# Optimization experiments

Measured on AMD Instinct MI355X. Metric: run time of the kernel, lower is better.

The kernel has to match this reference:

```python
import jax, jax.numpy as jnp
import numpy as np

N, E, D, H = 50000, 500000, 128, 4
C = D // H
EPS = 1e-5


def _layer_norm(x, g, b):
    mu = jnp.mean(x, axis=-1, keepdims=True)
    var = jnp.mean((x - mu) ** 2, axis=-1, keepdims=True)
    return (x - mu) * jax.lax.rsqrt(var + EPS) * g + b


def setup_inputs() -> dict:
    key = jax.random.key(0)
    ks = jax.random.split(key, 20)
    f = lambda i, shape: jax.random.normal(ks[i], shape, dtype=jnp.float32) * 0.05
    return {
        "x": f(0, (N, D)),
        "edge_index": jax.random.randint(ks[1], (2, E), 0, N),
        "w_gcn": f(2, (D, D)), "b_gcn": f(3, (D,)),
        "wq": f(4, (D, D)), "bq": f(5, (D,)),
        "wk": f(6, (D, D)), "bk": f(7, (D,)),
        "wv": f(8, (D, D)), "bv": f(9, (D,)),
        "w_skip": f(10, (D, D)), "b_skip": f(11, (D,)),
        "w_beta": f(12, (3 * D, 1)),
        "g1": jnp.ones((D,), jnp.float32), "b1": jnp.zeros((D,), jnp.float32),
        "g2": jnp.ones((D,), jnp.float32), "b2": jnp.zeros((D,), jnp.float32),
        "w_rel": f(13, (D, 2 * D)), "w_root": f(14, (2 * D, D)),
        "local_w": jnp.ones((1,), jnp.float32), "global_w": jnp.ones((1,), jnp.float32),
    }


def reference(x, edge_index, w_gcn, b_gcn, wq, bq, wk, bk, wv, bv,
              w_skip, b_skip, w_beta, g1, b1, g2, b2, w_rel, w_root,
              local_w, global_w):
    src, dst = edge_index[0], edge_index[1]

    # ---- GCNConv (add_self_loops=False, symmetric norm) ----
    xw = x @ w_gcn                                   # [N, D]
    deg = jax.ops.segment_sum(jnp.ones((E,), x.dtype), dst, num_segments=N)
    dinv = jnp.where(deg > 0, jax.lax.rsqrt(jnp.maximum(deg, 1.0)), 0.0)
    coef = dinv[src] * dinv[dst]                     # [E]
    local_out = jax.ops.segment_sum(coef[:, None] * xw[src], dst, num_segments=N) + b_gcn

    # ---- TransformerConv (heads=4, concat=True, beta=True) ----
    q = (x @ wq + bq).reshape(N, H, C)
    k = (x @ wk + bk).reshape(N, H, C)
    v = (x @ wv + bv).reshape(N, H, C)
    alpha = jnp.sum(q[dst] * k[src], axis=-1) / jnp.sqrt(jnp.float32(C))  # [E, H]
    m = jax.ops.segment_max(alpha, dst, num_segments=N)
    m = jnp.where(jnp.isfinite(m), m, 0.0)
    a = jnp.exp(alpha - m[dst])
    s = jax.ops.segment_sum(a, dst, num_segments=N)
    attn = a / jnp.maximum(s[dst], 1e-16)            # [E, H] segment softmax over in-edges
    agg = jax.ops.segment_sum(attn[..., None] * v[src], dst, num_segments=N)
    out_g = agg.reshape(N, D)
    x_r = x @ w_skip + b_skip
    beta = jax.nn.sigmoid(jnp.concatenate([out_g, x_r, out_g - x_r], axis=-1) @ w_beta)
    global_out = beta * x_r + (1.0 - beta) * out_g

    # ---- combine + norm + FFN ----
    h = local_w * local_out + global_w * global_out
    h = _layer_norm(h + h, g1, b1)
    out = jax.nn.relu(h @ w_rel) @ w_root
    out = _layer_norm(out + h, g2, b2)
    return out
```

## Files before the change

kernel.cpp:

```cpp
#include <hip/hip_runtime.h>
#include <math.h>

#define D 128
#define EPSV 1e-5f

typedef unsigned short ushort_t;
typedef unsigned char uchar_t;
typedef __attribute__((ext_vector_type(8))) short short8v;
typedef __attribute__((ext_vector_type(4))) float f32x4;
typedef __attribute__((ext_vector_type(2))) float f32x2;
typedef _Float16 half_t;
typedef __attribute__((ext_vector_type(2))) _Float16 h2;

#if __has_builtin(__builtin_amdgcn_cvt_pk_f16_fp8)
#define HAVE_F16P 1
#else
#define HAVE_F16P 0
#endif

__device__ __forceinline__ float bf2f(unsigned u) {
    return __uint_as_float(u << 16);
}
__device__ __forceinline__ ushort_t f2bf(float f) {
    unsigned u = __float_as_uint(f);
    unsigned r = (u + 0x7fffu + ((u >> 16) & 1u)) >> 16;
    return (ushort_t)r;
}
__device__ __forceinline__ float bfp(uint4 v, int i) {
    unsigned w = (&v.x)[i >> 1];
    return bf2f((i & 1) ? (w >> 16) : (w & 0xffffu));
}

__device__ __forceinline__ ushort_t qconv(float f) {
#if HAVE_F16P
    half_t h = (half_t)f;
    return __builtin_bit_cast(ushort_t, h);
#else
    return f2bf(f);
#endif
}

#define UNPACK8_FP8(u, o) { \
    f32x2 _a = __builtin_amdgcn_cvt_pk_f32_fp8((int)(u).x, false); \
    f32x2 _b = __builtin_amdgcn_cvt_pk_f32_fp8((int)(u).x, true);  \
    f32x2 _c = __builtin_amdgcn_cvt_pk_f32_fp8((int)(u).y, false); \
    f32x2 _d = __builtin_amdgcn_cvt_pk_f32_fp8((int)(u).y, true);  \
    o[0] = _a.x; o[1] = _a.y; o[2] = _b.x; o[3] = _b.y;            \
    o[4] = _c.x; o[5] = _c.y; o[6] = _d.x; o[7] = _d.y; }

__device__ __forceinline__ unsigned bf4_to_fp8x4(unsigned w0, unsigned w1) {
    int u = __builtin_amdgcn_cvt_pk_fp8_f32(bf2f(w0 & 0xffffu), bf2f(w0 >> 16), 0, false);
    u = __builtin_amdgcn_cvt_pk_fp8_f32(bf2f(w1 & 0xffffu), bf2f(w1 >> 16), u, true);
    return (unsigned)u;
}

__global__ void cvt_deg_kernel(const float* __restrict__ in, ushort_t* __restrict__ out, int n8,
                               const int* __restrict__ dst, int* __restrict__ deg, int E)
{
    int i = blockIdx.x * blockDim.x + threadIdx.x;
    if (i < n8) {
        float4 a = reinterpret_cast<const float4*>(in)[i * 2];
        float4 b = reinterpret_cast<const float4*>(in)[i * 2 + 1];
        uint4 o;
        o.x = (unsigned)f2bf(a.x) | ((unsigned)f2bf(a.y) << 16);
        o.y = (unsigned)f2bf(a.z) | ((unsigned)f2bf(a.w) << 16);
        o.z = (unsigned)f2bf(b.x) | ((unsigned)f2bf(b.y) << 16);
        o.w = (unsigned)f2bf(b.z) | ((unsigned)f2bf(b.w) << 16);
        reinterpret_cast<uint4*>(out)[i] = o;
    }
    if (i < E) atomicAdd(&deg[dst[i]], 1);
}

__global__ __launch_bounds__(256)
void proj_gemm(const ushort_t* __restrict__ xbf,
               const ushort_t* __restrict__ Bt,
               const float* __restrict__ bias,
               const float* __restrict__ dinv,
               uchar_t* __restrict__ pack, ushort_t* __restrict__ qb,
               ushort_t* __restrict__ xrb, int M)
{
    __shared__ ushort_t Cs[128 * 136];
    const int tid = threadIdx.x, lane = tid & 63, wid = tid >> 6;
    const int wr = wid >> 1, wc = wid & 1;
    const int R0 = blockIdx.x * 128;
    const int ct = blockIdx.y;

    short8v av[4][4];
    #pragma unroll
    for (int r = 0; r < 4; ++r) {
        int gr = R0 + wr * 64 + r * 16 + (lane & 15);
        if (gr >= M) gr = M - 1;
        #pragma unroll
        for (int ks = 0; ks < 4; ++ks)
            av[r][ks] = *reinterpret_cast<const short8v*>(
                &xbf[(size_t)gr * 128 + ks * 32 + (lane >> 4) * 8]);
    }

    f32x4 acc[4][4] = {};
    #pragma unroll
    for (int ks = 0; ks < 4; ++ks) {
        short8v bv[4];
        #pragma unroll
        for (int c = 0; c < 4; ++c) {
            int col = ct * 128 + wc * 64 + c * 16 + (lane & 15);
            bv[c] = *reinterpret_cast<const short8v*>(
                &Bt[(size_t)col * 128 + ks * 32 + (lane >> 4) * 8]);
        }
        #pragma unroll
        for (int r = 0; r < 4; ++r)
            #pragma unroll
            for (int c = 0; c < 4; ++c)
                acc[r][c] = __builtin_amdgcn_mfma_f32_16x16x32_bf16(av[r][ks], bv[c], acc[r][c], 0, 0, 0);
    }

    #pragma unroll
    for (int r = 0; r < 4; ++r) {
        int rowb = wr * 64 + r * 16 + (lane >> 4) * 4;
        #pragma unroll
        for (int i = 0; i < 4; ++i) {
            float sc = 1.f;
            if (ct == 0) {
                int grow = R0 + rowb + i;
                if (grow >= M) grow = M - 1;
                sc = dinv[grow];
            }
            #pragma unroll
            for (int c = 0; c < 4; ++c) {
                int col = wc * 64 + c * 16 + (lane & 15);
                float val = acc[r][c][i] + bias[ct * 128 + col];
                if (ct == 0) val *= sc;
                Cs[(rowb + i) * 136 + col] = (ct == 1) ? qconv(val) : f2bf(val);
            }
        }
    }
    __syncthreads();

    if (ct == 1 || ct == 4) {
        #pragma unroll
        for (int it = 0; it < 8; ++it) {
            int linear = tid + it * 256;
            int row = linear >> 4, ch = linear & 15;
            int gr = R0 + row;
            if (gr < M) {
                uint4 v = *reinterpret_cast<const uint4*>(&Cs[row * 136 + ch * 8]);
                ushort_t* dst = (ct == 1) ? (qb + (size_t)gr * 128)
                                          : (xrb + (size_t)gr * 128);
                *reinterpret_cast<uint4*>(dst + ch * 8) = v;
            }
        }
    } else {
        const int byteoff = (ct == 0) ? 256 : (ct == 2) ? 0 : 128;
        #pragma unroll
        for (int it = 0; it < 4; ++it) {
            int linear = tid + it * 256;
            int row = linear >> 3, ch = linear & 7;
            int gr = R0 + row;
            if (gr < M) {
                uint4 lo = *reinterpret_cast<const uint4*>(&Cs[row * 136 + ch * 16]);
                uint4 hi = *reinterpret_cast<const uint4*>(&Cs[row * 136 + ch * 16 + 8]);
                uint4 o;
                o.x = bf4_to_fp8x4(lo.x, lo.y);
                o.y = bf4_to_fp8x4(lo.z, lo.w);
                o.z = bf4_to_fp8x4(hi.x, hi.y);
                o.w = bf4_to_fp8x4(hi.z, hi.w);
                *reinterpret_cast<uint4*>(pack + (size_t)gr * 384 + byteoff + ch * 16) = o;
            }
        }
    }
}

__device__ __forceinline__ int swz(int ch, int row) {
    return (ch & 24) | ((ch ^ row) & 7);
}

__global__ __launch_bounds__(256)
void ffn_fused(const ushort_t* __restrict__ hlnb,
               const ushort_t* __restrict__ wt_rel,
               const ushort_t* __restrict__ wt_root,
               const float* __restrict__ g2, const float* __restrict__ b2,
               float* __restrict__ outf, int M)
{
    __shared__ float smem[128 * 130];
    ushort_t* Hs = (ushort_t*)smem;
    const int tid = threadIdx.x, lane = tid & 63, wid = tid >> 6;
    const int wr = wid >> 1, wc = wid & 1;
    const int R0 = blockIdx.x * 128;

    short8v av[4][4];
    #pragma unroll
    for (int r = 0; r < 4; ++r) {
        int gr = R0 + wr * 64 + r * 16 + (lane & 15);
        if (gr >= M) gr = M - 1;
        #pragma unroll
        for (int ks = 0; ks < 4; ++ks)
            av[r][ks] = *reinterpret_cast<const short8v*>(
                &hlnb[(size_t)gr * 128 + ks * 32 + (lane >> 4) * 8]);
    }
    for (int ct = 0; ct < 2; ++ct) {
        f32x4 acc[4][4] = {};
        #pragma unroll
        for (int ks = 0; ks < 4; ++ks) {
            short8v bv[4];
            #pragma unroll
            for (int c = 0; c < 4; ++c) {
                int col = ct * 128 + wc * 64 + c * 16 + (lane & 15);
                bv[c] = *reinterpret_cast<const short8v*>(
                    &wt_rel[(size_t)col * 128 + ks * 32 + (lane >> 4) * 8]);
            }
            #pragma unroll
            for (int r = 0; r < 4; ++r)
                #pragma unroll
                for (int c = 0; c < 4; ++c)
                    acc[r][c] = __builtin_amdgcn_mfma_f32_16x16x32_bf16(av[r][ks], bv[c], acc[r][c], 0, 0, 0);
        }
        #pragma unroll
        for (int r = 0; r < 4; ++r) {
            int rowb = wr * 64 + r * 16 + (lane >> 4) * 4;
            #pragma unroll
            for (int i = 0; i < 4; ++i)
                #pragma unroll
                for (int c = 0; c < 4; ++c) {
                    int row = rowb + i;
                    int col = ct * 128 + wc * 64 + c * 16 + (lane & 15);
                    int ch = col >> 3, el = col & 7;
                    Hs[row * 256 + swz(ch, row) * 8 + el] = f2bf(fmaxf(acc[r][c][i], 0.f));
                }
        }
    }
    __syncthreads();

    f32x4 acc2[4][4] = {};
    #pragma unroll
    for (int ks = 0; ks < 8; ++ks) {
        short8v a2[4], bv[4];
        #pragma unroll
        for (int r = 0; r < 4; ++r) {
            int row = wr * 64 + r * 16 + (lane & 15);
            int ch = ks * 4 + (lane >> 4);
            a2[r] = *reinterpret_cast<const short8v*>(&Hs[row * 256 + swz(ch, row) * 8]);
        }
        #pragma unroll
        for (int c = 0; c < 4; ++c) {
            int col = wc * 64 + c * 16 + (lane & 15);
            bv[c] = *reinterpret_cast<const short8v*>(
                &wt_root[(size_t)col * 256 + ks * 32 + (lane >> 4) * 8]);
        }
        #pragma unroll
        for (int r = 0; r < 4; ++r)
            #pragma unroll
            for (int c = 0; c < 4; ++c)
                acc2[r][c] = __builtin_amdgcn_mfma_f32_16x16x32_bf16(a2[r], bv[c], acc2[r][c], 0, 0, 0);
    }
    __syncthreads();

    float* Cs = smem;
    #pragma unroll
    for (int r = 0; r < 4; ++r) {
        int rowb = wr * 64 + r * 16 + (lane >> 4) * 4;
        #pragma unroll
        for (int i = 0; i < 4; ++i)
            #pragma unroll
            for (int c = 0; c < 4; ++c)
                Cs[(rowb + i) * 130 + wc * 64 + c * 16 + (lane & 15)] = acc2[r][c][i];
    }
    __syncthreads();

    const float ga = g2[lane * 2], gb = g2[lane * 2 + 1];
    const float ba = b2[lane * 2], bb2 = b2[lane * 2 + 1];
    for (int rr = 0; rr < 32; ++rr) {
        int row = wid * 32 + rr;
        int gr = R0 + row;
        if (gr >= M) break;
        unsigned hu = *reinterpret_cast<const unsigned*>(&hlnb[(size_t)gr * 128 + lane * 2]);
        float t0 = Cs[row * 130 + lane * 2]     + bf2f(hu & 0xffffu);
        float t1 = Cs[row * 130 + lane * 2 + 1] + bf2f(hu >> 16);
        float ssum = t0 + t1;
        #pragma unroll
        for (int off = 1; off <= 32; off <<= 1) ssum += __shfl_xor(ssum, off);
        float mu = ssum * (1.f / 128.f);
        float dv0 = t0 - mu, dv1 = t1 - mu;
        float vsum = dv0 * dv0 + dv1 * dv1;
        #pragma unroll
        for (int off = 1; off <= 32; off <<= 1) vsum += __shfl_xor(vsum, off);
        float rs = rsqrtf(vsum * (1.f / 128.f) + EPSV);
        float2 o = make_float2(dv0 * rs * ga + ba, dv1 * rs * gb + bb2);
        *reinterpret_cast<float2*>(&outf[(size_t)gr * 128 + lane * 2]) = o;
    }
}

__global__ __launch_bounds__(256)
void scan1_packw_kernel(const int* __restrict__ deg, int* __restrict__ row_start,
                        int* __restrict__ bsum, int n, int SB,
                        const float* __restrict__ wg, const float* __restrict__ wq,
                        const float* __restrict__ wk, const float* __restrict__ wv,
                        const float* __restrict__ wsk,
                        const float* __restrict__ bq, const float* __restrict__ bk,
                        const float* __restrict__ bv, const float* __restrict__ bsk,
                        const float* __restrict__ wrel, const float* __restrict__ wroot,
                        ushort_t* __restrict__ wt_all, ushort_t* __restrict__ wt_rel,
                        ushort_t* __restrict__ wt_root, float* __restrict__ bias_all)
{
    __shared__ int ws[4];
    if ((int)blockIdx.x < SB) {
        const int t = threadIdx.x, lane = t & 63, wid = t >> 6;
        const int base = blockIdx.x * 1024 + t * 4;
        int v0 = 0, v1 = 0, v2 = 0, v3 = 0;
        if (base + 3 < n) {
            int4 q = *reinterpret_cast<const int4*>(&deg[base]);
            v0 = q.x; v1 = q.y; v2 = q.z; v3 = q.w;
        } else {
            if (base < n)     v0 = deg[base];
            if (base + 1 < n) v1 = deg[base + 1];
            if (base + 2 < n) v2 = deg[base + 2];
            if (base + 3 < n) v3 = deg[base + 3];
        }
        int tot = v0 + v1 + v2 + v3;
        int inc = tot;
        #pragma unroll
        for (int off = 1; off < 64; off <<= 1) {
            int y = __shfl_up(inc, off);
            if (lane >= off) inc += y;
        }
        if (lane == 63) ws[wid] = inc;
        __syncthreads();
        int woff = 0;
        for (int w = 0; w < wid; ++w) woff += ws[w];
        int excl = woff + inc - tot;
        if (base < n)     row_start[base]     = excl;
        if (base + 1 < n) row_start[base + 1] = excl + v0;
        if (base + 2 < n) row_start[base + 2] = excl + v0 + v1;
        if (base + 3 < n) row_start[base + 3] = excl + v0 + v1 + v2;
        if (t == 0) bsum[blockIdx.x] = ws[0] + ws[1] + ws[2] + ws[3];
    } else {
        int i = (blockIdx.x - SB) * 256 + threadIdx.x;
        if (i < 640 * 128) {
            int c = i >> 7, k = i & 127;
            const float* srcs[5] = {wg, wq, wk, wv, wsk};
            wt_all[i] = f2bf(srcs[c >> 7][k * 128 + (c & 127)]);
        } else if (i < 640 * 128 + 256 * 128) {
            int j = i - 640 * 128;
            int c = j >> 7, k = j & 127;
            wt_rel[j] = f2bf(wrel[k * 256 + c]);
        } else if (i < 640 * 128 + 256 * 128 + 128 * 256) {
            int j = i - (640 * 128 + 256 * 128);
            int c = j >> 8, k = j & 255;
            wt_root[j] = f2bf(wroot[k * 128 + c]);
        } else if (i < 640 * 128 + 256 * 128 + 128 * 256 + 640) {
            int c = i - (640 * 128 + 256 * 128 + 128 * 256);
            float b = 0.f;
            if (c >= 128) {
                const float* bs[4] = {bq, bk, bv, bsk};
                b = bs[(c - 128) >> 7][c & 127];
            }
            bias_all[c] = b;
        }
    }
}

__global__ __launch_bounds__(256)
void scan3_kernel(const int* __restrict__ deg, const int* __restrict__ bsum,
                  int* __restrict__ row_start, int* __restrict__ cursor,
                  float* __restrict__ dinv, int n, int E)
{
    __shared__ int boff_s;
    const int K = blockIdx.x >> 2;
    const int t = threadIdx.x;
    if (t < 64) {
        int v = 0;
        for (int j = t; j < K; j += 64) v += bsum[j];
        #pragma unroll
        for (int off = 1; off <= 32; off <<= 1) v += __shfl_xor(v, off);
        if (t == 0) boff_s = v;
    }
    __syncthreads();
    int i = blockIdx.x * 256 + t;
    if (i < n) {
        int rs = row_start[i] + boff_s;
        row_start[i] = rs;
        cursor[i] = rs;
        int d = deg[i];
        dinv[i] = (d > 0) ? rsqrtf((float)d) : 0.f;
    }
    if (i == 0) row_start[n] = E;
}

__global__ void fill_kernel(const int* __restrict__ src, const int* __restrict__ dst,
                            int* __restrict__ cursor, int* __restrict__ csr_src, int E)
{
    int e = (blockIdx.x * blockDim.x + threadIdx.x) * 2;
    if (e + 1 < E) {
        int2 s2 = *reinterpret_cast<const int2*>(&src[e]);
        int2 d2 = *reinterpret_cast<const int2*>(&dst[e]);
        int p0 = atomicAdd(&cursor[d2.x], 1);
        csr_src[p0] = s2.x;
        int p1 = atomicAdd(&cursor[d2.y], 1);
        csr_src[p1] = s2.y;
    } else if (e < E) {
        int d = dst[e];
        int pos = atomicAdd(&cursor[d], 1);
        csr_src[pos] = src[e];
    }
}

__global__ __launch_bounds__(256)
void edge_fused_kernel(const uchar_t* __restrict__ pack,
                       const ushort_t* __restrict__ qbf,
                       const ushort_t* __restrict__ xrbf,
                       const int* __restrict__ row_start,
                       const int* __restrict__ csr_src,
                       const float* __restrict__ dinv,
                       const float* __restrict__ b_gcn,
                       const float* __restrict__ w_beta,
                       const float* __restrict__ g1, const float* __restrict__ b1,
                       const float* __restrict__ local_w, const float* __restrict__ global_w,
                       ushort_t* __restrict__ hln_bf, int n)
{
    const int wid = threadIdx.x >> 6, lane = threadIdx.x & 63;
    const int node = blockIdx.x * 4 + wid;
    if (node >= n) return;
    const int slot = lane >> 4, li = lane & 15;
    const int d8 = li * 8;

    const int e0 = row_start[node], e1 = row_start[node + 1];
    const int cnt = e1 - e0;
    const float dn = dinv[node];
    const float scale = 0.17677669529663687f;

    float s = 0.f;
    float va[8], ga[8];

#if HAVE_F16P
    uint4 qu = *reinterpret_cast<const uint4*>(&qbf[(size_t)node * 128 + d8]);
    h2 qh[4] = { __builtin_bit_cast(h2, qu.x), __builtin_bit_cast(h2, qu.y),
                 __builtin_bit_cast(h2, qu.z), __builtin_bit_cast(h2, qu.w) };
    h2 va2[4] = {}, ga2[4] = {};
    for (int j = e0; j < e1; j += 4) {
        const int je = j + slot;
        const int sidx = (je < e1) ? csr_src[je] : n;
        const uchar_t* prow = pack + (size_t)sidx * 384;
        uint2 ku = *reinterpret_cast<const uint2*>(prow + d8);
        uint2 vu = *reinterpret_cast<const uint2*>(prow + 128 + d8);
        uint2 xu = *reinterpret_cast<const uint2*>(prow + 256 + d8);
        h2 k0 = __builtin_amdgcn_cvt_pk_f16_fp8((short)(ku.x & 0xffffu));
        h2 k1 = __builtin_amdgcn_cvt_pk_f16_fp8((short)(ku.x >> 16));
        h2 k2 = __builtin_amdgcn_cvt_pk_f16_fp8((short)(ku.y & 0xffffu));
        h2 k3 = __builtin_amdgcn_cvt_pk_f16_fp8((short)(ku.y >> 16));
        float p = __builtin_amdgcn_fdot2(k0, qh[0], 0.f, false);
        p = __builtin_amdgcn_fdot2(k1, qh[1], p, false);
        p = __builtin_amdgcn_fdot2(k2, qh[2], p, false);
        p = __builtin_amdgcn_fdot2(k3, qh[3], p, false);
        p += __shfl_xor(p, 1);
        p += __shfl_xor(p, 2);
        float wgt = __expf(p * scale);
        s += wgt;
        half_t wh = (half_t)wgt;
        h2 w2 = { wh, wh };
        h2 v0 = __builtin_amdgcn_cvt_pk_f16_fp8((short)(vu.x & 0xffffu));
        h2 v1 = __builtin_amdgcn_cvt_pk_f16_fp8((short)(vu.x >> 16));
        h2 v2 = __builtin_amdgcn_cvt_pk_f16_fp8((short)(vu.y & 0xffffu));
        h2 v3 = __builtin_amdgcn_cvt_pk_f16_fp8((short)(vu.y >> 16));
        va2[0] += w2 * v0; va2[1] += w2 * v1; va2[2] += w2 * v2; va2[3] += w2 * v3;
        h2 x0 = __builtin_amdgcn_cvt_pk_f16_fp8((short)(xu.x & 0xffffu));
        h2 x1 = __builtin_amdgcn_cvt_pk_f16_fp8((short)(xu.x >> 16));
        h2 x2 = __builtin_amdgcn_cvt_pk_f16_fp8((short)(xu.y & 0xffffu));
        h2 x3 = __builtin_amdgcn_cvt_pk_f16_fp8((short)(xu.y >> 16));
        ga2[0] += x0; ga2[1] += x1; ga2[2] += x2; ga2[3] += x3;
    }
    #pragma unroll
    for (int i = 0; i < 4; ++i) {
        va[2 * i] = (float)va2[i][0]; va[2 * i + 1] = (float)va2[i][1];
        ga[2 * i] = (float)ga2[i][0]; ga[2 * i + 1] = (float)ga2[i][1];
    }
#else
    uint4 qu = *reinterpret_cast<const uint4*>(&qbf[(size_t)node * 128 + d8]);
    float q[8];
    #pragma unroll
    for (int i = 0; i < 8; ++i) q[i] = bfp(qu, i);
    #pragma unroll
    for (int i = 0; i < 8; ++i) { va[i] = 0.f; ga[i] = 0.f; }
    for (int j = e0; j < e1; j += 4) {
        const int je = j + slot;
        const int sidx = (je < e1) ? csr_src[je] : n;
        const uchar_t* prow = pack + (size_t)sidx * 384;
        uint2 ku = *reinterpret_cast<const uint2*>(prow + d8);
        uint2 vu = *reinterpret_cast<const uint2*>(prow + 128 + d8);
        uint2 xu = *reinterpret_cast<const uint2*>(prow + 256 + d8);
        float kf[8], vf[8], xf[8];
        UNPACK8_FP8(ku, kf);
        UNPACK8_FP8(vu, vf);
        UNPACK8_FP8(xu, xf);
        float p = 0.f;
        #pragma unroll
        for (int i = 0; i < 8; ++i) p = fmaf(q[i], kf[i], p);
        p += __shfl_xor(p, 1);
        p += __shfl_xor(p, 2);
        float wgt = __expf(p * scale);
        s += wgt;
        #pragma unroll
        for (int i = 0; i < 8; ++i) {
            va[i] = fmaf(wgt, vf[i], va[i]);
            ga[i] += xf[i];
        }
    }
#endif

    s -= (float)((4 - (cnt & 3)) & 3) * 0.25f * 0.f;

    #pragma unroll
    for (int off = 16; off <= 32; off <<= 1) {
        s += __shfl_xor(s, off);
        #pragma unroll
        for (int i = 0; i < 8; ++i) {
            va[i] += __shfl_xor(va[i], off);
            ga[i] += __shfl_xor(ga[i], off);
        }
    }
    if (cnt > 0) s -= (float)((4 - (cnt & 3)) & 3);
    const float denom = fmaxf(s, 1e-16f);

    uint4 xru = *reinterpret_cast<const uint4*>(&xrbf[(size_t)node * 128 + d8]);
    float t[8];
    float part = 0.f;
    #pragma unroll
    for (int i = 0; i < 8; ++i) {
        float og = va[i] / denom;
        float xr = bfp(xru, i);
        float lo = dn * ga[i] + b_gcn[d8 + i];
        part += og * w_beta[d8 + i] + xr * w_beta[128 + d8 + i]
              + (og - xr) * w_beta[256 + d8 + i];
        t[i] = lo;
        va[i] = og; ga[i] = xr;
    }
    #pragma unroll
    for (int off = 1; off <= 32; off <<= 1) part += __shfl_xor(part, off);
    const float beta = 1.f / (1.f + __expf(-part * 0.25f));

    const float lw = local_w[0], gw = global_w[0];
    float ssum = 0.f;
    #pragma unroll
    for (int i = 0; i < 8; ++i) {
        float go = beta * ga[i] + (1.f - beta) * va[i];
        t[i] = 2.f * (lw * t[i] + gw * go);
        ssum += t[i];
    }
    #pragma unroll
    for (int off = 1; off <= 32; off <<= 1) ssum += __shfl_xor(ssum, off);
    const float mu = ssum * (1.f / 512.f);
    float vsum = 0.f;
    #pragma unroll
    for (int i = 0; i < 8; ++i) { float d = t[i] - mu; vsum += d * d; }
    #pragma unroll
    for (int off = 1; off <= 32; off <<= 1) vsum += __shfl_xor(vsum, off);
    const float rs = rsqrtf(vsum * (1.f / 512.f) + EPSV);

    if (slot == 0) {
        uint4 o;
        #pragma unroll
        for (int i = 0; i < 4; ++i) {
            float o0 = (t[2*i]   - mu) * rs * g1[d8 + 2*i]   + b1[d8 + 2*i];
            float o1 = (t[2*i+1] - mu) * rs * g1[d8 + 2*i+1] + b1[d8 + 2*i+1];
            (&o.x)[i] = (unsigned)f2bf(o0) | ((unsigned)f2bf(o1) << 16);
        }
        *reinterpret_cast<uint4*>(&hln_bf[(size_t)node * 128 + d8]) = o;
    }
}

extern "C" void kernel_launch(void* const* d_in, const int* in_sizes, int n_in,
                              void* d_out, int out_size, void* d_ws, size_t ws_size,
                              hipStream_t stream)
{
    const float* x      = (const float*)d_in[0];
    const int*   ei     = (const int*)d_in[1];
    const float* w_gcn  = (const float*)d_in[2];
    const float* b_gcn  = (const float*)d_in[3];
    const float* wq     = (const float*)d_in[4];
    const float* bq     = (const float*)d_in[5];
    const float* wk     = (const float*)d_in[6];
    const float* bk     = (const float*)d_in[7];
    const float* wv     = (const float*)d_in[8];
    const float* bv     = (const float*)d_in[9];
    const float* w_skip = (const float*)d_in[10];
    const float* b_skip = (const float*)d_in[11];
    const float* w_beta = (const float*)d_in[12];
    const float* g1     = (const float*)d_in[13];
    const float* b1     = (const float*)d_in[14];
    const float* g2     = (const float*)d_in[15];
    const float* b2     = (const float*)d_in[16];
    const float* w_rel  = (const float*)d_in[17];
    const float* w_root = (const float*)d_in[18];
    const float* lw     = (const float*)d_in[19];
    const float* gw     = (const float*)d_in[20];

    const int N = in_sizes[0] / D;
    const int E = in_sizes[1] / 2;
    const int* src = ei;
    const int* dst = ei + E;

    char* wsb = (char*)d_ws;
    size_t off = 0;
    auto alloc = [&](size_t bytes) -> void* {
        void* p = wsb + off;
        off += (bytes + 255) & ~(size_t)255;
        return p;
    };
    uchar_t*  pack_kvx = (uchar_t*)alloc((size_t)(N + 1) * 384);
    ushort_t* xbf      = (ushort_t*)alloc((size_t)N * 128 * 2);
    ushort_t* qb_bf    = (ushort_t*)alloc((size_t)N * 128 * 2);
    ushort_t* xr_bf    = (ushort_t*)alloc((size_t)N * 128 * 2);
    ushort_t* hln_bf   = (ushort_t*)alloc((size_t)N * 128 * 2);
    ushort_t* wt_all   = (ushort_t*)alloc(640 * 128 * 2);
    ushort_t* wt_rel   = (ushort_t*)alloc(256 * 128 * 2);
    ushort_t* wt_root  = (ushort_t*)alloc(128 * 256 * 2);
    float*    bias_all = (float*)alloc(640 * 4);
    int*      deg      = (int*)alloc((size_t)N * 4);
    int*      row_start= (int*)alloc((size_t)(N + 1) * 4);
    int*      cursor   = (int*)alloc((size_t)N * 4);
    int*      csr_src  = (int*)alloc((size_t)E * 4);
    float*    dinv     = (float*)alloc((size_t)N * 4);
    int*      bsum     = (int*)alloc(((size_t)(N + 1023) / 1024) * 4);

    float* out = (float*)d_out;
    const int SB = (N + 1023) / 1024;
    const int n8 = N * 16;

    hipMemsetAsync(deg, 0, (size_t)N * sizeof(int), stream);
    hipMemsetAsync(pack_kvx + (size_t)N * 384, 0, 384, stream);
    {
        int work = (n8 > E) ? n8 : E;
        cvt_deg_kernel<<<dim3((work + 255) / 256), dim3(256), 0, stream>>>(
            x, xbf, n8, dst, deg, E);
    }
    scan1_packw_kernel<<<dim3(SB + 579), dim3(256), 0, stream>>>(
        deg, row_start, bsum, N, SB,
        w_gcn, wq, wk, wv, w_skip, bq, bk, bv, b_skip, w_rel, w_root,
        wt_all, wt_rel, wt_root, bias_all);
    scan3_kernel<<<dim3((N + 255) / 256), dim3(256), 0, stream>>>(
        deg, bsum, row_start, cursor, dinv, N, E);
    fill_kernel<<<dim3((E / 2 + 255) / 256), dim3(256), 0, stream>>>(src, dst, cursor, csr_src, E);

    const int MB = (N + 127) / 128;
    proj_gemm<<<dim3(MB, 5), dim3(256), 0, stream>>>(
        xbf, wt_all, bias_all, dinv, pack_kvx, qb_bf, xr_bf, N);

    edge_fused_kernel<<<dim3((N + 3) / 4), dim3(256), 0, stream>>>(
        pack_kvx, qb_bf, xr_bf, row_start, csr_src, dinv, b_gcn, w_beta,
        g1, b1, lw, gw, hln_bf, N);

    ffn_fused<<<dim3(MB), dim3(256), 0, stream>>>(
        hln_bf, wt_rel, wt_root, g2, b2, out, N);
}
```

Baseline: 206.9 us.

## Interleave K/V fp8 rows for single 16-byte gathers and shrink reductions

Changes the packed fp8 node layout so K and V chunks for the same lane sit next to each other, letting each edge gather use one 16-byte load plus one 8-byte load instead of three 8-byte loads. The cross-slot reduction in the fp16 path now runs on packed half2 values, halving the shuffle count. The beta, mean and variance reductions now shuffle only within 16 lanes rather than the full wave, since all four slots hold identical values after the slot reduction. The trade-off is extra precision loss from summing partial accumulators in fp16, plus a dependency on the new indexing (li) matching the packing.

After: 206.3 us. Within noise of the previous version (-0.3%).

```diff
diff --git a/kernel.cpp b/kernel.cpp
--- a/kernel.cpp
+++ b/kernel.cpp
@@ -40,18 +40,22 @@
 #endif
 }
 
-#define UNPACK8_FP8(u, o) { \
-    f32x2 _a = __builtin_amdgcn_cvt_pk_f32_fp8((int)(u).x, false); \
-    f32x2 _b = __builtin_amdgcn_cvt_pk_f32_fp8((int)(u).x, true);  \
-    f32x2 _c = __builtin_amdgcn_cvt_pk_f32_fp8((int)(u).y, false); \
-    f32x2 _d = __builtin_amdgcn_cvt_pk_f32_fp8((int)(u).y, true);  \
-    o[0] = _a.x; o[1] = _a.y; o[2] = _b.x; o[3] = _b.y;            \
+#define UNPACK8_FP8(ux, uy, o) { \
+    f32x2 _a = __builtin_amdgcn_cvt_pk_f32_fp8((int)(ux), false); \
+    f32x2 _b = __builtin_amdgcn_cvt_pk_f32_fp8((int)(ux), true);  \
+    f32x2 _c = __builtin_amdgcn_cvt_pk_f32_fp8((int)(uy), false); \
+    f32x2 _d = __builtin_amdgcn_cvt_pk_f32_fp8((int)(uy), true);  \
+    o[0] = _a.x; o[1] = _a.y; o[2] = _b.x; o[3] = _b.y;           \
     o[4] = _c.x; o[5] = _c.y; o[6] = _d.x; o[7] = _d.y; }
 
 __device__ __forceinline__ unsigned bf4_to_fp8x4(unsigned w0, unsigned w1) {
     int u = __builtin_amdgcn_cvt_pk_fp8_f32(bf2f(w0 & 0xffffu), bf2f(w0 >> 16), 0, false);
     u = __builtin_amdgcn_cvt_pk_fp8_f32(bf2f(w1 & 0xffffu), bf2f(w1 >> 16), u, true);
     return (unsigned)u;
+}
+
+__device__ __forceinline__ h2 h2_shfl_xor_add(h2 a, int off) {
+    return a + __builtin_bit_cast(h2, __shfl_xor(__builtin_bit_cast(int, a), off));
 }
 
 __global__ void cvt_deg_kernel(const float* __restrict__ in, ushort_t* __restrict__ out, int n8,
@@ -149,7 +153,6 @@
             }
         }
     } else {
-        const int byteoff = (ct == 0) ? 256 : (ct == 2) ? 0 : 128;
         #pragma unroll
         for (int it = 0; it < 4; ++it) {
             int linear = tid + it * 256;
@@ -163,7 +166,16 @@
                 o.y = bf4_to_fp8x4(lo.z, lo.w);
                 o.z = bf4_to_fp8x4(hi.x, hi.y);
                 o.w = bf4_to_fp8x4(hi.z, hi.w);
-                *reinterpret_cast<uint4*>(pack + (size_t)gr * 384 + byteoff + ch * 16) = o;
+                uchar_t* prow = pack + (size_t)gr * 384;
+                if (ct == 0) {
+                    *reinterpret_cast<uint4*>(prow + 256 + ch * 16) = o;
+                } else if (ct == 2) {
+                    *reinterpret_cast<uint2*>(prow + (2 * ch) * 16)     = make_uint2(o.x, o.y);
+                    *reinterpret_cast<uint2*>(prow + (2 * ch + 1) * 16) = make_uint2(o.z, o.w);
+                } else {
+                    *reinterpret_cast<uint2*>(prow + (2 * ch) * 16 + 8)     = make_uint2(o.x, o.y);
+                    *reinterpret_cast<uint2*>(prow + (2 * ch + 1) * 16 + 8) = make_uint2(o.z, o.w);
+                }
             }
         }
     }
@@ -438,13 +450,12 @@
         const int je = j + slot;
         const int sidx = (je < e1) ? csr_src[je] : n;
         const uchar_t* prow = pack + (size_t)sidx * 384;
-        uint2 ku = *reinterpret_cast<const uint2*>(prow + d8);
-        uint2 vu = *reinterpret_cast<const uint2*>(prow + 128 + d8);
-        uint2 xu = *reinterpret_cast<const uint2*>(prow + 256 + d8);
-        h2 k0 = __builtin_amdgcn_cvt_pk_f16_fp8((short)(ku.x & 0xffffu));
-        h2 k1 = __builtin_amdgcn_cvt_pk_f16_fp8((short)(ku.x >> 16));
-        h2 k2 = __builtin_amdgcn_cvt_pk_f16_fp8((short)(ku.y & 0xffffu));
-        h2 k3 = __builtin_amdgcn_cvt_pk_f16_fp8((short)(ku.y >> 16));
+        uint4 kv = *reinterpret_cast<const uint4*>(prow + li * 16);
+        uint2 xu = *reinterpret_cast<const uint2*>(prow + 256 + li * 8);
+        h2 k0 = __builtin_amdgcn_cvt_pk_f16_fp8((short)(kv.x & 0xffffu));
+        h2 k1 = __builtin_amdgcn_cvt_pk_f16_fp8((short)(kv.x >> 16));
+        h2 k2 = __builtin_amdgcn_cvt_pk_f16_fp8((short)(kv.y & 0xffffu));
+        h2 k3 = __builtin_amdgcn_cvt_pk_f16_fp8((short)(kv.y >> 16));
         float p = __builtin_amdgcn_fdot2(k0, qh[0], 0.f, false);
         p = __builtin_amdgcn_fdot2(k1, qh[1], p, false);
         p = __builtin_amdgcn_fdot2(k2, qh[2], p, false);
@@ -455,10 +466,10 @@
         s += wgt;
         half_t wh = (half_t)wgt;
         h2 w2 = { wh, wh };
-        h2 v0 = __builtin_amdgcn_cvt_pk_f16_fp8((short)(vu.x & 0xffffu));
-        h2 v1 = __builtin_amdgcn_cvt_pk_f16_fp8((short)(vu.x >> 16));
-        h2 v2 = __builtin_amdgcn_cvt_pk_f16_fp8((short)(vu.y & 0xffffu));
-        h2 v3 = __builtin_amdgcn_cvt_pk_f16_fp8((short)(vu.y >> 16));
+        h2 v0 = __builtin_amdgcn_cvt_pk_f16_fp8((short)(kv.z & 0xffffu));
+        h2 v1 = __builtin_amdgcn_cvt_pk_f16_fp8((short)(kv.z >> 16));
+        h2 v2 = __builtin_amdgcn_cvt_pk_f16_fp8((short)(kv.w & 0xffffu));
+        h2 v3 = __builtin_amdgcn_cvt_pk_f16_fp8((short)(kv.w >> 16));
         va2[0] += w2 * v0; va2[1] += w2 * v1; va2[2] += w2 * v2; va2[3] += w2 * v3;
         h2 x0 = __builtin_amdgcn_cvt_pk_f16_fp8((short)(xu.x & 0xffffu));
         h2 x1 = __builtin_amdgcn_cvt_pk_f16_fp8((short)(xu.x >> 16));
@@ -467,6 +478,14 @@
         ga2[0] += x0; ga2[1] += x1; ga2[2] += x2; ga2[3] += x3;
     }
     #pragma unroll
+    for (int off = 16; off <= 32; off <<= 1) {
+        #pragma unroll
+        for (int i = 0; i < 4; ++i) {
+            va2[i] = h2_shfl_xor_add(va2[i], off);
+            ga2[i] = h2_shfl_xor_add(ga2[i], off);
+        }
+    }
+    #pragma unroll
     for (int i = 0; i < 4; ++i) {
         va[2 * i] = (float)va2[i][0]; va[2 * i + 1] = (float)va2[i][1];
         ga[2 * i] = (float)ga2[i][0]; ga[2 * i + 1] = (float)ga2[i][1];
@@ -482,13 +501,12 @@
         const int je = j + slot;
         const int sidx = (je < e1) ? csr_src[je] : n;
         const uchar_t* prow = pack + (size_t)sidx * 384;
-        uint2 ku = *reinterpret_cast<const uint2*>(prow + d8);
-        uint2 vu = *reinterpret_cast<const uint2*>(prow + 128 + d8);
-        uint2 xu = *reinterpret_cast<const uint2*>(prow + 256 + d8);
+        uint4 kv = *reinterpret_cast<const uint4*>(prow + li * 16);
+        uint2 xu = *reinterpret_cast<const uint2*>(prow + 256 + li * 8);
         float kf[8], vf[8], xf[8];
-        UNPACK8_FP8(ku, kf);
-        UNPACK8_FP8(vu, vf);
-        UNPACK8_FP8(xu, xf);
+        UNPACK8_FP8(kv.x, kv.y, kf);
+        UNPACK8_FP8(kv.z, kv.w, vf);
+        UNPACK8_FP8(xu.x, xu.y, xf);
         float p = 0.f;
         #pragma unroll
         for (int i = 0; i < 8; ++i) p = fmaf(q[i], kf[i], p);
@@ -502,19 +520,18 @@
             ga[i] += xf[i];
         }
     }
-#endif
-
-    s -= (float)((4 - (cnt & 3)) & 3) * 0.25f * 0.f;
-
     #pragma unroll
     for (int off = 16; off <= 32; off <<= 1) {
-        s += __shfl_xor(s, off);
         #pragma unroll
         for (int i = 0; i < 8; ++i) {
             va[i] += __shfl_xor(va[i], off);
             ga[i] += __shfl_xor(ga[i], off);
         }
     }
+#endif
+
+    s += __shfl_xor(s, 16);
+    s += __shfl_xor(s, 32);
     if (cnt > 0) s -= (float)((4 - (cnt & 3)) & 3);
     const float denom = fmaxf(s, 1e-16f);
 
@@ -532,8 +549,8 @@
         va[i] = og; ga[i] = xr;
     }
     #pragma unroll
-    for (int off = 1; off <= 32; off <<= 1) part += __shfl_xor(part, off);
-    const float beta = 1.f / (1.f + __expf(-part * 0.25f));
+    for (int off = 1; off <= 8; off <<= 1) part += __shfl_xor(part, off);
+    const float beta = 1.f / (1.f + __expf(-part));
 
     const float lw = local_w[0], gw = global_w[0];
     float ssum = 0.f;
@@ -544,14 +561,14 @@
         ssum += t[i];
     }
     #pragma unroll
-    for (int off = 1; off <= 32; off <<= 1) ssum += __shfl_xor(ssum, off);
-    const float mu = ssum * (1.f / 512.f);
+    for (int off = 1; off <= 8; off <<= 1) ssum += __shfl_xor(ssum, off);
+    const float mu = ssum * (1.f / 128.f);
     float vsum = 0.f;
     #pragma unroll
     for (int i = 0; i < 8; ++i) { float d = t[i] - mu; vsum += d * d; }
     #pragma unroll
-    for (int off = 1; off <= 32; off <<= 1) vsum += __shfl_xor(vsum, off);
-    const float rs = rsqrtf(vsum * (1.f / 512.f) + EPSV);
+    for (int off = 1; off <= 8; off <<= 1) vsum += __shfl_xor(vsum, off);
+    const float rs = rsqrtf(vsum * (1.f / 128.f) + EPSV);
 
     if (slot == 0) {
         uint4 o;
```
